# Kernel tuning notes

Measured on AMD Instinct MI355X. Metric: run time of the kernel, lower is better.

Reference implementation:

```python
import jax, jax.numpy as jnp
import numpy as np

B, T, L, H, W = 8, 30000, 6, 128, 128
D_IN, C_DIM, HID, Z_DIM = 3, 32, 256, 128
MAX_DIM = 0.55


def setup_inputs() -> dict:
    key = jax.random.key(0)
    ks = jax.random.split(key, 12)
    p = jax.random.uniform(ks[0], (B, T, D_IN), dtype=jnp.float32)
    z = jax.random.normal(ks[1], (B, Z_DIM), dtype=jnp.float32)
    c = jax.random.normal(ks[2], (B, L, H, W, C_DIM), dtype=jnp.float32)
    # camera-like matrices: small rotation rows so projected coords stay in [-1, 1]
    C_mat = (jax.random.uniform(ks[3], (B, L, 4, 3), dtype=jnp.float32) - 0.5) * 0.3
    C_mat = C_mat.at[:, :, 3, :].set(1.0)  # row used as projection denominator
    fc_p_w = jax.random.normal(ks[4], (HID, D_IN), dtype=jnp.float32) * 0.1
    fc_p_b = jnp.zeros((HID,), jnp.float32)
    blk0_w0 = jax.random.normal(ks[5], (C_DIM, HID), dtype=jnp.float32) * 0.05
    blk0_b0 = jnp.zeros((C_DIM,), jnp.float32)
    blk0_w1 = jax.random.normal(ks[6], (C_DIM, C_DIM), dtype=jnp.float32) * 0.1
    blk0_b1 = jnp.zeros((C_DIM,), jnp.float32)
    blk0_ws = jax.random.normal(ks[7], (C_DIM, HID), dtype=jnp.float32) * 0.05
    blk_w0 = jax.random.normal(ks[8], (4, C_DIM, C_DIM), dtype=jnp.float32) * 0.1
    blk_b0 = jnp.zeros((4, C_DIM), jnp.float32)
    blk_w1 = jax.random.normal(ks[9], (4, C_DIM, C_DIM), dtype=jnp.float32) * 0.1
    blk_b1 = jnp.zeros((4, C_DIM), jnp.float32)
    fc_out_w = jax.random.normal(ks[10], (1, C_DIM), dtype=jnp.float32) * 0.1
    fc_out_b = jnp.zeros((1,), jnp.float32)
    return dict(p=p, z=z, c=c, C_mat=C_mat, fc_p_w=fc_p_w, fc_p_b=fc_p_b,
                blk0_w0=blk0_w0, blk0_b0=blk0_b0, blk0_w1=blk0_w1, blk0_b1=blk0_b1,
                blk0_ws=blk0_ws, blk_w0=blk_w0, blk_b0=blk_b0, blk_w1=blk_w1,
                blk_b1=blk_b1, fc_out_w=fc_out_w, fc_out_b=fc_out_b)


def _bilinear(p, c, C_mat):
    # p: [B,T,3], c: [B,L,H,W,D], C_mat: [B,L,4,3]
    Bb, Ll, Hh, Ww, Dd = c.shape
    interval = 2.0 / (Hh - 1)
    pp = p / MAX_DIM
    # proj[b,l,t,i] = sum_j C_mat[b,l,i,j] * pp[b,t,j]
    proj = jnp.einsum('blij,btj->blti', C_mat[:, :, :3, :], pp)
    denom = C_mat[:, :, 3, 0] + 0.05                      # [B,L]
    proj = proj / denom[:, :, None, None]
    xy = (proj[..., :2] + 1.0) / interval                 # [B,L,T,2]
    x, y = xy[..., 0], xy[..., 1]
    x0f, x1f = jnp.floor(x), jnp.ceil(x)
    y0f, y1f = jnp.floor(y), jnp.ceil(y)
    dx = (x1f - x)[..., None]                             # [B,L,T,1]
    dy = (y1f - y)[..., None]
    x0 = jnp.clip(x0f.astype(jnp.int32), 0, Hh - 1)
    x1 = jnp.clip(x1f.astype(jnp.int32), 0, Hh - 1)
    y0 = jnp.clip(y0f.astype(jnp.int32), 0, Ww - 1)
    y1 = jnp.clip(y1f.astype(jnp.int32), 0, Ww - 1)
    bi = jnp.arange(Bb)[:, None, None]
    li = jnp.arange(Ll)[None, :, None]
    f11 = c[bi, li, x0, y0]                               # [B,L,T,D]
    f12 = c[bi, li, x1, y0]
    f21 = c[bi, li, x0, y1]
    f22 = c[bi, li, x1, y1]
    interp = (f11 * dx * dy + f12 * (1 - dx) * dy
              + f21 * dx * (1 - dy) + f22 * (1 - dx) * (1 - dy))
    return interp.sum(axis=1)                             # sum over views -> [B,T,D]


def reference(p, z, c, C_mat, fc_p_w, fc_p_b, blk0_w0, blk0_b0, blk0_w1, blk0_b1,
              blk0_ws, blk_w0, blk_b0, blk_w1, blk_b1, fc_out_w, fc_out_b):
    feat = _bilinear(p, c, C_mat)                         # [B,T,32]
    net = p @ fc_p_w.T + fc_p_b                           # 1x1 conv == linear, [B,T,256]
    # block0 (256 -> 32, with linear shortcut)
    h = jax.nn.relu(net) @ blk0_w0.T + blk0_b0
    dx_ = jax.nn.relu(h) @ blk0_w1.T + blk0_b1
    net = net @ blk0_ws.T + dx_
    net = net + feat
    # blocks 1..4 (32 -> 32, identity shortcut)
    for i in range(4):
        h = jax.nn.relu(net) @ blk_w0[i].T + blk_b0[i]
        net = net + (jax.nn.relu(h) @ blk_w1[i].T + blk_b1[i])
        net = net + feat
    out = jax.nn.relu(net) @ fc_out_w.T + fc_out_b        # [B,T,1]
    return out[..., 0]                                    # [B,T]
```

## Files before the change

kernel.cpp:

```cpp
#include <hip/hip_runtime.h>

#define NB 8
#define NT 30000
#define NL 6
#define NC 32
#define NHID 256

typedef _Float16 f16;
typedef f16 half8 __attribute__((ext_vector_type(8)));
typedef float floatx4 __attribute__((ext_vector_type(4)));

__device__ __forceinline__ int permrow(int m) {
    return 8 * ((m & 15) >> 2) + 4 * (m >> 4) + (m & 3);
}

__global__ void fold_kernel(const float* __restrict__ ws, const float* __restrict__ fpw,
                            const float* __restrict__ fpb, floatx4* __restrict__ out) {
    int i = threadIdx.x;
    if (i < NC) {
        float m0 = 0.f, m1 = 0.f, m2 = 0.f, v = 0.f;
        for (int k = 0; k < NHID; k++) {
            float w = ws[i * NHID + k];
            m0 = fmaf(w, fpw[k * 3 + 0], m0);
            m1 = fmaf(w, fpw[k * 3 + 1], m1);
            m2 = fmaf(w, fpw[k * 3 + 2], m2);
            v  = fmaf(w, fpb[k], v);
        }
        out[i] = floatx4{m0, m1, m2, v};
    }
}

__device__ __forceinline__ void gemm32(const f16* __restrict__ wmat, int i16, int q,
                                       const float in[8], floatx4& o0, floatx4& o1) {
    half8 bf;
    #pragma unroll
    for (int j = 0; j < 8; j++) bf[j] = (f16)fmaxf(in[j], 0.f);
    half8 a0 = *(const half8*)(wmat + i16 * 40 + q * 8);
    half8 a1 = *(const half8*)(wmat + (16 + i16) * 40 + q * 8);
    o0 = __builtin_amdgcn_mfma_f32_16x16x32_f16(a0, bf, o0, 0, 0, 0);
    o1 = __builtin_amdgcn_mfma_f32_16x16x32_f16(a1, bf, o1, 0, 0, 0);
}

__launch_bounds__(256, 3)
__global__ void decoder_kernel(
    const float* __restrict__ p, const float* __restrict__ c, const float* __restrict__ Cm,
    const float* __restrict__ fpw, const float* __restrict__ fpb,
    const float* __restrict__ b0w0, const float* __restrict__ b0b0,
    const float* __restrict__ b0w1, const float* __restrict__ b0b1,
    const float* __restrict__ bw0, const float* __restrict__ bb0,
    const float* __restrict__ bw1, const float* __restrict__ bb1,
    const float* __restrict__ fow, const float* __restrict__ fob,
    const floatx4* __restrict__ fold, float* __restrict__ out)
{
    __shared__ __align__(16) f16 s_w0A[32 * 288];
    __shared__ __align__(16) f16 s_wA[9 * 32 * 40];
    __shared__ floatx4 s_fcp[288];
    __shared__ floatx4 s_fold[36];
    __shared__ __align__(16) float s_b0b0[32], s_b0b1[32], s_fow[32];
    __shared__ __align__(16) float s_bb0f[128], s_bb1f[128];
    __shared__ float s_cam[NL][8];
    __shared__ float s_fob;

    const int tid = threadIdx.x;
    const int b = blockIdx.y;

    for (int idx = tid; idx < 32 * 256; idx += 256) {
        int m = idx >> 8, k = idx & 255;
        s_w0A[m * 288 + k] = (f16)b0w0[permrow(m) * 256 + k];
    }
    for (int idx = tid; idx < 9 * 1024; idx += 256) {
        int mi = idx >> 10, rem = idx & 1023;
        int m = rem >> 5, k = rem & 31;
        int pm = permrow(m);
        float v;
        if (mi == 0) v = b0w1[pm * 32 + k];
        else {
            int mat = mi - 1, bi = mat >> 1;
            v = (mat & 1) ? bw1[(bi * 32 + pm) * 32 + k] : bw0[(bi * 32 + pm) * 32 + k];
        }
        s_wA[mi * 1280 + m * 40 + k] = (f16)v;
    }
    {
        int k = tid;
        s_fcp[k + (k >> 3)] = floatx4{fpw[k * 3 + 0], fpw[k * 3 + 1], fpw[k * 3 + 2], fpb[k]};
    }
    if (tid < 32) {
        s_b0b0[tid] = b0b0[tid];
        s_b0b1[tid] = b0b1[tid];
        s_fow[tid]  = fow[tid];
        s_fold[tid + (tid >> 3)] = fold[tid];
    }
    if (tid >= 64 && tid < 192) {
        int j = tid - 64;
        s_bb0f[j] = bb0[j];
        s_bb1f[j] = bb1[j];
    }
    if (tid == 0) s_fob = fob[0];
    if (tid >= 192 && tid < 192 + NL) {
        int l = tid - 192;
        const float* cm = Cm + ((size_t)b * NL + l) * 12;
        float denom = cm[9] + 0.05f;
        float s = 63.5f / (0.55f * denom);
        s_cam[l][0] = cm[0] * s; s_cam[l][1] = cm[1] * s; s_cam[l][2] = cm[2] * s;
        s_cam[l][3] = cm[3] * s; s_cam[l][4] = cm[4] * s; s_cam[l][5] = cm[5] * s;
    }
    __syncthreads();

    const int lane = tid & 63;
    const int wv = tid >> 6;
    const int q = lane >> 4;
    const int i16 = lane & 15;
    const int t = blockIdx.x * 64 + wv * 16 + i16;
    const int tc = min(t, NT - 1);

    const float* pp = p + ((size_t)b * NT + tc) * 3;
    float px = pp[0], py = pp[1], pz = pp[2];

    float feat[8];
    #pragma unroll
    for (int u = 0; u < 8; u++) feat[u] = 0.f;
    const float* cq = c + (((size_t)b * NL) << 19) + q * 8;
    #pragma unroll 1
    for (int l = 0; l < NL; l++) {
        float x = s_cam[l][0] * px + s_cam[l][1] * py + s_cam[l][2] * pz + 63.5f;
        float y = s_cam[l][3] * px + s_cam[l][4] * py + s_cam[l][5] * pz + 63.5f;
        float x0f = floorf(x), x1f = ceilf(x);
        float y0f = floorf(y), y1f = ceilf(y);
        float dxw = x1f - x, dyw = y1f - y;
        int x0 = min(max((int)x0f, 0), 127);
        int x1 = min(max((int)x1f, 0), 127);
        int y0 = min(max((int)y0f, 0), 127);
        int y1 = min(max((int)y1f, 0), 127);
        const float* base = cq + ((size_t)l << 19);
        const floatx4* f11 = (const floatx4*)(base + (size_t)((x0 << 7) + y0) * 32);
        const floatx4* f12 = (const floatx4*)(base + (size_t)((x1 << 7) + y0) * 32);
        const floatx4* f21 = (const floatx4*)(base + (size_t)((x0 << 7) + y1) * 32);
        const floatx4* f22 = (const floatx4*)(base + (size_t)((x1 << 7) + y1) * 32);
        float w11 = dxw * dyw;
        float w12 = (1.f - dxw) * dyw;
        float w21 = dxw * (1.f - dyw);
        float w22 = (1.f - dxw) * (1.f - dyw);
        floatx4 a0 = f11[0], a1 = f11[1];
        floatx4 b0v = f12[0], b1v = f12[1];
        floatx4 c0 = f21[0], c1 = f21[1];
        floatx4 d0 = f22[0], d1 = f22[1];
        #pragma unroll
        for (int u = 0; u < 4; u++) {
            feat[u]     += a0[u] * w11 + b0v[u] * w12 + c0[u] * w21 + d0[u] * w22;
            feat[4 + u] += a1[u] * w11 + b1v[u] * w12 + c1[u] * w21 + d1[u] * w22;
        }
    }

    floatx4 acc0 = *(const floatx4*)&s_b0b0[q * 8];
    floatx4 acc1 = *(const floatx4*)&s_b0b0[q * 8 + 4];
    const f16* w0row0 = s_w0A + i16 * 288;
    const f16* w0row1 = s_w0A + (16 + i16) * 288;
    #pragma unroll 2
    for (int cch = 0; cch < 8; cch++) {
        half8 bf;
        #pragma unroll
        for (int j = 0; j < 8; j++) {
            floatx4 w = s_fcp[cch * 36 + q * 9 + j];
            bf[j] = (f16)fmaxf(w[0] * px + w[1] * py + w[2] * pz + w[3], 0.f);
        }
        half8 a0 = *(const half8*)(w0row0 + cch * 32 + q * 8);
        half8 a1 = *(const half8*)(w0row1 + cch * 32 + q * 8);
        acc0 = __builtin_amdgcn_mfma_f32_16x16x32_f16(a0, bf, acc0, 0, 0, 0);
        acc1 = __builtin_amdgcn_mfma_f32_16x16x32_f16(a1, bf, acc1, 0, 0, 0);
    }

    float hbuf[8];
    #pragma unroll
    for (int r = 0; r < 4; r++) { hbuf[r] = acc0[r]; hbuf[4 + r] = acc1[r]; }
    floatx4 n0 = *(const floatx4*)&s_b0b1[q * 8];
    floatx4 n1 = *(const floatx4*)&s_b0b1[q * 8 + 4];
    gemm32(s_wA, i16, q, hbuf, n0, n1);

    float st[8];
    #pragma unroll
    for (int j = 0; j < 8; j++) {
        floatx4 f = s_fold[q * 9 + j];
        float sc = f[0] * px + f[1] * py + f[2] * pz + f[3];
        st[j] = ((j < 4) ? n0[j] : n1[j - 4]) + sc + feat[j];
    }

    #pragma unroll
    for (int bk = 0; bk < 4; bk++) {
        floatx4 h0 = *(const floatx4*)&s_bb0f[bk * 32 + q * 8];
        floatx4 h1 = *(const floatx4*)&s_bb0f[bk * 32 + q * 8 + 4];
        gemm32(s_wA + (1 + 2 * bk) * 1280, i16, q, st, h0, h1);
        float hb[8];
        #pragma unroll
        for (int r = 0; r < 4; r++) { hb[r] = h0[r]; hb[4 + r] = h1[r]; }
        floatx4 d0 = *(const floatx4*)&s_bb1f[bk * 32 + q * 8];
        floatx4 d1 = *(const floatx4*)&s_bb1f[bk * 32 + q * 8 + 4];
        gemm32(s_wA + (2 + 2 * bk) * 1280, i16, q, hb, d0, d1);
        #pragma unroll
        for (int j = 0; j < 8; j++)
            st[j] += ((j < 4) ? d0[j] : d1[j - 4]) + feat[j];
    }

    floatx4 fw0 = *(const floatx4*)&s_fow[q * 8];
    floatx4 fw1 = *(const floatx4*)&s_fow[q * 8 + 4];
    float o = 0.f;
    #pragma unroll
    for (int r = 0; r < 4; r++)
        o += fmaxf(st[r], 0.f) * fw0[r] + fmaxf(st[4 + r], 0.f) * fw1[r];
    o += __shfl_xor(o, 16);
    o += __shfl_xor(o, 32);
    if (q == 0 && t < NT) out[(size_t)b * NT + t] = o + s_fob;
}

extern "C" void kernel_launch(void* const* d_in, const int* in_sizes, int n_in,
                              void* d_out, int out_size, void* d_ws, size_t ws_size,
                              hipStream_t stream) {
    const float* p    = (const float*)d_in[0];
    const float* c    = (const float*)d_in[2];
    const float* Cm   = (const float*)d_in[3];
    const float* fpw  = (const float*)d_in[4];
    const float* fpb  = (const float*)d_in[5];
    const float* b0w0 = (const float*)d_in[6];
    const float* b0b0 = (const float*)d_in[7];
    const float* b0w1 = (const float*)d_in[8];
    const float* b0b1 = (const float*)d_in[9];
    const float* b0ws = (const float*)d_in[10];
    const float* bw0  = (const float*)d_in[11];
    const float* bb0  = (const float*)d_in[12];
    const float* bw1  = (const float*)d_in[13];
    const float* bb1  = (const float*)d_in[14];
    const float* fow  = (const float*)d_in[15];
    const float* fob  = (const float*)d_in[16];
    floatx4* fold = (floatx4*)d_ws;

    fold_kernel<<<1, 64, 0, stream>>>(b0ws, fpw, fpb, fold);

    dim3 grid((NT + 63) / 64, NB);
    decoder_kernel<<<grid, 256, 0, stream>>>(p, c, Cm, fpw, fpb,
                                             b0w0, b0b0, b0w1, b0b1,
                                             bw0, bb0, bw1, bb1,
                                             fow, fob, fold, (float*)d_out);
}
```

Measured before the change: 307.4 us.

## Compute fc_p layer on MFMA, swizzle LDS weights, and loop four point groups per block

The first 3->256 linear layer moves from scalar FMAs to MFMA, using a padded K=4 weight tile in fp16 (x, y, z, bias). Each block now processes 256 points over four iterations, which amortizes the shared-memory weight staging. The unpadded LDS weight arrays use an XOR swizzle, conversions use packed cvt_pkrtz, occupancy is raised to 4 blocks per SM, and the fold kernel is parallelized across 256 threads. Feeding the first-layer inputs and weights through fp16 costs accuracy in that layer, and the extra loop iterations add register pressure.

```diff
diff --git a/kernel.cpp b/kernel.cpp
--- a/kernel.cpp
+++ b/kernel.cpp
@@ -8,40 +8,65 @@
 
 typedef _Float16 f16;
 typedef f16 half8 __attribute__((ext_vector_type(8)));
+typedef f16 half4v __attribute__((ext_vector_type(4)));
+typedef f16 half2v __attribute__((ext_vector_type(2)));
 typedef float floatx4 __attribute__((ext_vector_type(4)));
 
 __device__ __forceinline__ int permrow(int m) {
     return 8 * ((m & 15) >> 2) + 4 * (m >> 4) + (m & 3);
 }
 
+__device__ __forceinline__ half2v cvt2(float a, float b) {
+    auto t = __builtin_amdgcn_cvt_pkrtz(a, b);
+    return *(half2v*)&t;
+}
+
+__device__ __forceinline__ half8 relupack(const float in[8]) {
+    union { half8 v; half2v p[4]; } u;
+    u.p[0] = cvt2(fmaxf(in[0], 0.f), fmaxf(in[1], 0.f));
+    u.p[1] = cvt2(fmaxf(in[2], 0.f), fmaxf(in[3], 0.f));
+    u.p[2] = cvt2(fmaxf(in[4], 0.f), fmaxf(in[5], 0.f));
+    u.p[3] = cvt2(fmaxf(in[6], 0.f), fmaxf(in[7], 0.f));
+    return u.v;
+}
+
 __global__ void fold_kernel(const float* __restrict__ ws, const float* __restrict__ fpw,
                             const float* __restrict__ fpb, floatx4* __restrict__ out) {
-    int i = threadIdx.x;
-    if (i < NC) {
-        float m0 = 0.f, m1 = 0.f, m2 = 0.f, v = 0.f;
-        for (int k = 0; k < NHID; k++) {
-            float w = ws[i * NHID + k];
-            m0 = fmaf(w, fpw[k * 3 + 0], m0);
-            m1 = fmaf(w, fpw[k * 3 + 1], m1);
-            m2 = fmaf(w, fpw[k * 3 + 2], m2);
-            v  = fmaf(w, fpb[k], v);
-        }
-        out[i] = floatx4{m0, m1, m2, v};
-    }
-}
-
-__device__ __forceinline__ void gemm32(const f16* __restrict__ wmat, int i16, int q,
+    __shared__ floatx4 s_part[8][32];
+    int tid = threadIdx.x;
+    int i = tid & 31, kc = tid >> 5;
+    const float* wrow = ws + i * 256 + kc * 32;
+    const float* pw = fpw + kc * 96;
+    const float* pb = fpb + kc * 32;
+    floatx4 acc = {};
+    #pragma unroll 8
+    for (int k = 0; k < 32; k++) {
+        float w = wrow[k];
+        acc[0] = fmaf(w, pw[k * 3 + 0], acc[0]);
+        acc[1] = fmaf(w, pw[k * 3 + 1], acc[1]);
+        acc[2] = fmaf(w, pw[k * 3 + 2], acc[2]);
+        acc[3] = fmaf(w, pb[k], acc[3]);
+    }
+    s_part[kc][i] = acc;
+    __syncthreads();
+    if (kc == 0) {
+        floatx4 s = s_part[0][i];
+        #pragma unroll
+        for (int j = 1; j < 8; j++) s += s_part[j][i];
+        out[i] = s;
+    }
+}
+
+__device__ __forceinline__ void gemm32(const f16* __restrict__ wmat, int soff0, int soff1,
                                        const float in[8], floatx4& o0, floatx4& o1) {
-    half8 bf;
-    #pragma unroll
-    for (int j = 0; j < 8; j++) bf[j] = (f16)fmaxf(in[j], 0.f);
-    half8 a0 = *(const half8*)(wmat + i16 * 40 + q * 8);
-    half8 a1 = *(const half8*)(wmat + (16 + i16) * 40 + q * 8);
+    half8 bf = relupack(in);
+    half8 a0 = *(const half8*)(wmat + soff0);
+    half8 a1 = *(const half8*)(wmat + soff1);
     o0 = __builtin_amdgcn_mfma_f32_16x16x32_f16(a0, bf, o0, 0, 0, 0);
     o1 = __builtin_amdgcn_mfma_f32_16x16x32_f16(a1, bf, o1, 0, 0, 0);
 }
 
-__launch_bounds__(256, 3)
+__launch_bounds__(256, 4)
 __global__ void decoder_kernel(
     const float* __restrict__ p, const float* __restrict__ c, const float* __restrict__ Cm,
     const float* __restrict__ fpw, const float* __restrict__ fpb,
@@ -52,9 +77,9 @@
     const float* __restrict__ fow, const float* __restrict__ fob,
     const floatx4* __restrict__ fold, float* __restrict__ out)
 {
-    __shared__ __align__(16) f16 s_w0A[32 * 288];
-    __shared__ __align__(16) f16 s_wA[9 * 32 * 40];
-    __shared__ floatx4 s_fcp[288];
+    __shared__ __align__(16) f16 s_w0A[32 * 256];
+    __shared__ __align__(16) f16 s_wA[9 * 32 * 32];
+    __shared__ __align__(16) f16 s_hA[256 * 4];
     __shared__ floatx4 s_fold[36];
     __shared__ __align__(16) float s_b0b0[32], s_b0b1[32], s_fow[32];
     __shared__ __align__(16) float s_bb0f[128], s_bb1f[128];
@@ -64,25 +89,50 @@
     const int tid = threadIdx.x;
     const int b = blockIdx.y;
 
-    for (int idx = tid; idx < 32 * 256; idx += 256) {
-        int m = idx >> 8, k = idx & 255;
-        s_w0A[m * 288 + k] = (f16)b0w0[permrow(m) * 256 + k];
-    }
-    for (int idx = tid; idx < 9 * 1024; idx += 256) {
-        int mi = idx >> 10, rem = idx & 1023;
-        int m = rem >> 5, k = rem & 31;
+    {
+        int m = tid >> 3, seg = tid & 7;
+        const float* src = b0w0 + permrow(m) * 256 + seg * 32;
+        f16* dst = s_w0A + m * 256;
+        int sw = m & 7;
+        #pragma unroll
+        for (int ci = 0; ci < 4; ci++) {
+            int cidx = seg * 4 + ci;
+            floatx4 f0 = *(const floatx4*)(src + ci * 8);
+            floatx4 f1 = *(const floatx4*)(src + ci * 8 + 4);
+            half8 h;
+            #pragma unroll
+            for (int j = 0; j < 4; j++) { h[j] = (f16)f0[j]; h[4 + j] = (f16)f1[j]; }
+            *(half8*)(dst + ((cidx ^ sw) << 3)) = h;
+        }
+    }
+    for (int r = tid; r < 288; r += 256) {
+        int mi = r >> 5, m = r & 31;
         int pm = permrow(m);
-        float v;
-        if (mi == 0) v = b0w1[pm * 32 + k];
+        const float* src;
+        if (mi == 0) src = b0w1 + pm * 32;
         else {
             int mat = mi - 1, bi = mat >> 1;
-            v = (mat & 1) ? bw1[(bi * 32 + pm) * 32 + k] : bw0[(bi * 32 + pm) * 32 + k];
-        }
-        s_wA[mi * 1280 + m * 40 + k] = (f16)v;
+            src = ((mat & 1) ? bw1 : bw0) + (bi * 32 + pm) * 32;
+        }
+        f16* dst = s_wA + mi * 1024 + m * 32;
+        int sw = (m >> 1) & 3;
+        #pragma unroll
+        for (int ci = 0; ci < 4; ci++) {
+            floatx4 f0 = *(const floatx4*)(src + ci * 8);
+            floatx4 f1 = *(const floatx4*)(src + ci * 8 + 4);
+            half8 h;
+            #pragma unroll
+            for (int j = 0; j < 4; j++) { h[j] = (f16)f0[j]; h[4 + j] = (f16)f1[j]; }
+            *(half8*)(dst + ((ci ^ sw) << 3)) = h;
+        }
     }
     {
-        int k = tid;
-        s_fcp[k + (k >> 3)] = floatx4{fpw[k * 3 + 0], fpw[k * 3 + 1], fpw[k * 3 + 2], fpb[k]};
+        int cch = tid >> 5, m = tid & 31;
+        int h = cch * 32 + permrow(m);
+        half4v v;
+        v[0] = (f16)fpw[h * 3 + 0]; v[1] = (f16)fpw[h * 3 + 1];
+        v[2] = (f16)fpw[h * 3 + 2]; v[3] = (f16)fpb[h];
+        *(half4v*)(s_hA + tid * 4) = v;
     }
     if (tid < 32) {
         s_b0b0[tid] = b0b0[tid];
@@ -110,105 +160,131 @@
     const int wv = tid >> 6;
     const int q = lane >> 4;
     const int i16 = lane & 15;
-    const int t = blockIdx.x * 64 + wv * 16 + i16;
-    const int tc = min(t, NT - 1);
-
-    const float* pp = p + ((size_t)b * NT + tc) * 3;
-    float px = pp[0], py = pp[1], pz = pp[2];
-
-    float feat[8];
-    #pragma unroll
-    for (int u = 0; u < 8; u++) feat[u] = 0.f;
+
+    const int sw0 = i16 & 7;
+    const f16* w0r0 = s_w0A + i16 * 256;
+    const f16* w0r1 = s_w0A + (16 + i16) * 256;
+    const int qsw = (q ^ ((i16 >> 1) & 3)) << 3;
+    const int soff0 = i16 * 32 + qsw;
+    const int soff1 = (16 + i16) * 32 + qsw;
+    const f16* hr0 = s_hA + i16 * 4;
+    const f16* hr1 = s_hA + (16 + i16) * 4;
     const float* cq = c + (((size_t)b * NL) << 19) + q * 8;
+
     #pragma unroll 1
-    for (int l = 0; l < NL; l++) {
-        float x = s_cam[l][0] * px + s_cam[l][1] * py + s_cam[l][2] * pz + 63.5f;
-        float y = s_cam[l][3] * px + s_cam[l][4] * py + s_cam[l][5] * pz + 63.5f;
-        float x0f = floorf(x), x1f = ceilf(x);
-        float y0f = floorf(y), y1f = ceilf(y);
-        float dxw = x1f - x, dyw = y1f - y;
-        int x0 = min(max((int)x0f, 0), 127);
-        int x1 = min(max((int)x1f, 0), 127);
-        int y0 = min(max((int)y0f, 0), 127);
-        int y1 = min(max((int)y1f, 0), 127);
-        const float* base = cq + ((size_t)l << 19);
-        const floatx4* f11 = (const floatx4*)(base + (size_t)((x0 << 7) + y0) * 32);
-        const floatx4* f12 = (const floatx4*)(base + (size_t)((x1 << 7) + y0) * 32);
-        const floatx4* f21 = (const floatx4*)(base + (size_t)((x0 << 7) + y1) * 32);
-        const floatx4* f22 = (const floatx4*)(base + (size_t)((x1 << 7) + y1) * 32);
-        float w11 = dxw * dyw;
-        float w12 = (1.f - dxw) * dyw;
-        float w21 = dxw * (1.f - dyw);
-        float w22 = (1.f - dxw) * (1.f - dyw);
-        floatx4 a0 = f11[0], a1 = f11[1];
-        floatx4 b0v = f12[0], b1v = f12[1];
-        floatx4 c0 = f21[0], c1 = f21[1];
-        floatx4 d0 = f22[0], d1 = f22[1];
-        #pragma unroll
-        for (int u = 0; u < 4; u++) {
-            feat[u]     += a0[u] * w11 + b0v[u] * w12 + c0[u] * w21 + d0[u] * w22;
-            feat[4 + u] += a1[u] * w11 + b1v[u] * w12 + c1[u] * w21 + d1[u] * w22;
-        }
-    }
-
-    floatx4 acc0 = *(const floatx4*)&s_b0b0[q * 8];
-    floatx4 acc1 = *(const floatx4*)&s_b0b0[q * 8 + 4];
-    const f16* w0row0 = s_w0A + i16 * 288;
-    const f16* w0row1 = s_w0A + (16 + i16) * 288;
-    #pragma unroll 2
-    for (int cch = 0; cch < 8; cch++) {
-        half8 bf;
+    for (int g = 0; g < 4; g++) {
+        const int t = blockIdx.x * 256 + (g * 4 + wv) * 16 + i16;
+        const int tc = min(t, NT - 1);
+        const float* pp = p + ((size_t)b * NT + tc) * 3;
+        float px = pp[0], py = pp[1], pz = pp[2];
+
+        floatx4 fe0 = {}, fe1 = {};
+        #pragma unroll 2
+        for (int l = 0; l < NL; l++) {
+            float x = s_cam[l][0] * px + s_cam[l][1] * py + s_cam[l][2] * pz + 63.5f;
+            float y = s_cam[l][3] * px + s_cam[l][4] * py + s_cam[l][5] * pz + 63.5f;
+            float x0f = floorf(x), x1f = ceilf(x);
+            float y0f = floorf(y), y1f = ceilf(y);
+            float dxw = x1f - x, dyw = y1f - y;
+            int x0 = min(max((int)x0f, 0), 127);
+            int x1 = min(max((int)x1f, 0), 127);
+            int y0 = min(max((int)y0f, 0), 127);
+            int y1 = min(max((int)y1f, 0), 127);
+            const float* base = cq + ((size_t)l << 19);
+            const floatx4* f11 = (const floatx4*)(base + (size_t)((x0 << 7) + y0) * 32);
+            const floatx4* f12 = (const floatx4*)(base + (size_t)((x1 << 7) + y0) * 32);
+            const floatx4* f21 = (const floatx4*)(base + (size_t)((x0 << 7) + y1) * 32);
+            const floatx4* f22 = (const floatx4*)(base + (size_t)((x1 << 7) + y1) * 32);
+            float w11 = dxw * dyw;
+            float w12 = (1.f - dxw) * dyw;
+            float w21 = dxw * (1.f - dyw);
+            float w22 = (1.f - dxw) * (1.f - dyw);
+            floatx4 a0 = f11[0], a1 = f11[1];
+            floatx4 b0v = f12[0], b1v = f12[1];
+            floatx4 c0 = f21[0], c1 = f21[1];
+            floatx4 d0 = f22[0], d1 = f22[1];
+            fe0 += a0 * w11 + b0v * w12 + c0 * w21 + d0 * w22;
+            fe1 += a1 * w11 + b1v * w12 + c1 * w21 + d1 * w22;
+        }
+        float feat[8];
+        #pragma unroll
+        for (int r = 0; r < 4; r++) { feat[r] = fe0[r]; feat[4 + r] = fe1[r]; }
+
+        half8 bp;
+        {
+            union { half8 v; half2v p2[4]; } u;
+            half2v z = {};
+            u.p2[0] = (q == 0) ? cvt2(px, py) : z;
+            u.p2[1] = (q == 0) ? cvt2(pz, 1.0f) : z;
+            u.p2[2] = z; u.p2[3] = z;
+            bp = u.v;
+        }
+        floatx4 acc0 = *(const floatx4*)&s_b0b0[q * 8];
+        floatx4 acc1 = *(const floatx4*)&s_b0b0[q * 8 + 4];
+        #pragma unroll
+        for (int cch = 0; cch < 8; cch++) {
+            half4v lo = *(const half4v*)(hr0 + cch * 128);
+            half4v hi = *(const half4v*)(hr1 + cch * 128);
+            half8 alo, ahi;
+            #pragma unroll
+            for (int j = 0; j < 4; j++) {
+                alo[j] = lo[j]; alo[4 + j] = lo[j];
+                ahi[j] = hi[j]; ahi[4 + j] = hi[j];
+            }
+            floatx4 hz = {};
+            floatx4 h0 = __builtin_amdgcn_mfma_f32_16x16x32_f16(alo, bp, hz, 0, 0, 0);
+            floatx4 h1 = __builtin_amdgcn_mfma_f32_16x16x32_f16(ahi, bp, hz, 0, 0, 0);
+            float hv[8];
+            #pragma unroll
+            for (int r = 0; r < 4; r++) { hv[r] = h0[r]; hv[4 + r] = h1[r]; }
+            half8 bf = relupack(hv);
+            half8 a0 = *(const half8*)(w0r0 + ((((cch << 2) | q) ^ sw0) << 3));
+            half8 a1 = *(const half8*)(w0r1 + ((((cch << 2) | q) ^ sw0) << 3));
+            acc0 = __builtin_amdgcn_mfma_f32_16x16x32_f16(a0, bf, acc0, 0, 0, 0);
+            acc1 = __builtin_amdgcn_mfma_f32_16x16x32_f16(a1, bf, acc1, 0, 0, 0);
+        }
+
+        float hbuf[8];
+        #pragma unroll
+        for (int r = 0; r < 4; r++) { hbuf[r] = acc0[r]; hbuf[4 + r] = acc1[r]; }
+        floatx4 n0 = *(const floatx4*)&s_b0b1[q * 8];
+        floatx4 n1 = *(const floatx4*)&s_b0b1[q * 8 + 4];
+        gemm32(s_wA, soff0, soff1, hbuf, n0, n1);
+
+        float st[8];
         #pragma unroll
         for (int j = 0; j < 8; j++) {
-            floatx4 w = s_fcp[cch * 36 + q * 9 + j];
-            bf[j] = (f16)fmaxf(w[0] * px + w[1] * py + w[2] * pz + w[3], 0.f);
-        }
-        half8 a0 = *(const half8*)(w0row0 + cch * 32 + q * 8);
-        half8 a1 = *(const half8*)(w0row1 + cch * 32 + q * 8);
-        acc0 = __builtin_amdgcn_mfma_f32_16x16x32_f16(a0, bf, acc0, 0, 0, 0);
-        acc1 = __builtin_amdgcn_mfma_f32_16x16x32_f16(a1, bf, acc1, 0, 0, 0);
-    }
-
-    float hbuf[8];
-    #pragma unroll
-    for (int r = 0; r < 4; r++) { hbuf[r] = acc0[r]; hbuf[4 + r] = acc1[r]; }
-    floatx4 n0 = *(const floatx4*)&s_b0b1[q * 8];
-    floatx4 n1 = *(const floatx4*)&s_b0b1[q * 8 + 4];
-    gemm32(s_wA, i16, q, hbuf, n0, n1);
-
-    float st[8];
-    #pragma unroll
-    for (int j = 0; j < 8; j++) {
-        floatx4 f = s_fold[q * 9 + j];
-        float sc = f[0] * px + f[1] * py + f[2] * pz + f[3];
-        st[j] = ((j < 4) ? n0[j] : n1[j - 4]) + sc + feat[j];
-    }
-
-    #pragma unroll
-    for (int bk = 0; bk < 4; bk++) {
-        floatx4 h0 = *(const floatx4*)&s_bb0f[bk * 32 + q * 8];
-        floatx4 h1 = *(const floatx4*)&s_bb0f[bk * 32 + q * 8 + 4];
-        gemm32(s_wA + (1 + 2 * bk) * 1280, i16, q, st, h0, h1);
-        float hb[8];
-        #pragma unroll
-        for (int r = 0; r < 4; r++) { hb[r] = h0[r]; hb[4 + r] = h1[r]; }
-        floatx4 d0 = *(const floatx4*)&s_bb1f[bk * 32 + q * 8];
-        floatx4 d1 = *(const floatx4*)&s_bb1f[bk * 32 + q * 8 + 4];
-        gemm32(s_wA + (2 + 2 * bk) * 1280, i16, q, hb, d0, d1);
-        #pragma unroll
-        for (int j = 0; j < 8; j++)
-            st[j] += ((j < 4) ? d0[j] : d1[j - 4]) + feat[j];
-    }
-
-    floatx4 fw0 = *(const floatx4*)&s_fow[q * 8];
-    floatx4 fw1 = *(const floatx4*)&s_fow[q * 8 + 4];
-    float o = 0.f;
-    #pragma unroll
-    for (int r = 0; r < 4; r++)
-        o += fmaxf(st[r], 0.f) * fw0[r] + fmaxf(st[4 + r], 0.f) * fw1[r];
-    o += __shfl_xor(o, 16);
-    o += __shfl_xor(o, 32);
-    if (q == 0 && t < NT) out[(size_t)b * NT + t] = o + s_fob;
+            floatx4 f = s_fold[q * 9 + j];
+            float sc = f[0] * px + f[1] * py + f[2] * pz + f[3];
+            st[j] = ((j < 4) ? n0[j] : n1[j - 4]) + sc + feat[j];
+        }
+
+        #pragma unroll
+        for (int bk = 0; bk < 4; bk++) {
+            floatx4 h0 = *(const floatx4*)&s_bb0f[bk * 32 + q * 8];
+            floatx4 h1 = *(const floatx4*)&s_bb0f[bk * 32 + q * 8 + 4];
+            gemm32(s_wA + (1 + 2 * bk) * 1024, soff0, soff1, st, h0, h1);
+            float hb[8];
+            #pragma unroll
+            for (int r = 0; r < 4; r++) { hb[r] = h0[r]; hb[4 + r] = h1[r]; }
+            floatx4 d0 = *(const floatx4*)&s_bb1f[bk * 32 + q * 8];
+            floatx4 d1 = *(const floatx4*)&s_bb1f[bk * 32 + q * 8 + 4];
+            gemm32(s_wA + (2 + 2 * bk) * 1024, soff0, soff1, hb, d0, d1);
+            #pragma unroll
+            for (int j = 0; j < 8; j++)
+                st[j] += ((j < 4) ? d0[j] : d1[j - 4]) + feat[j];
+        }
+
+        floatx4 fw0 = *(const floatx4*)&s_fow[q * 8];
+        floatx4 fw1 = *(const floatx4*)&s_fow[q * 8 + 4];
+        float o = 0.f;
+        #pragma unroll
+        for (int r = 0; r < 4; r++)
+            o += fmaxf(st[r], 0.f) * fw0[r] + fmaxf(st[4 + r], 0.f) * fw1[r];
+        o += __shfl_xor(o, 16);
+        o += __shfl_xor(o, 32);
+        if (q == 0 && t < NT) out[(size_t)b * NT + t] = o + s_fob;
+    }
 }
 
 extern "C" void kernel_launch(void* const* d_in, const int* in_sizes, int n_in,
@@ -232,9 +308,9 @@
     const float* fob  = (const float*)d_in[16];
     floatx4* fold = (floatx4*)d_ws;
 
-    fold_kernel<<<1, 64, 0, stream>>>(b0ws, fpw, fpb, fold);
-
-    dim3 grid((NT + 63) / 64, NB);
+    fold_kernel<<<1, 256, 0, stream>>>(b0ws, fpw, fpb, fold);
+
+    dim3 grid((NT + 255) / 256, NB);
     decoder_kernel<<<grid, 256, 0, stream>>>(p, c, Cm, fpw, fpb,
                                              b0w0, b0b0, b0w1, b0b1,
                                              bw0, bb0, bw1, bb1,
```

After: 467.8 us. 1.52x slower.
